# Optimization experiments

Measured on AMD Instinct MI355X. Metric: run time of the kernel, lower is better.

The kernel has to match this reference:

```python
import jax, jax.numpy as jnp
import numpy as np

N_NODES = 100000
N_EDGES = 1600000
C = 64


def _spline_conv(x, src, dst, u, w, root, bias, n_nodes):
    """SplineConv, dim=1, kernel_size=2, degree=1, open spline, aggr='mean'.

    For K=2, degree=1, pseudo u in [0,1]: basis = (1-u) on knot 0, u on knot 1.
    message_e = (1-u_e) * x[src_e] @ w[0] + u_e * x[src_e] @ w[1]
    Compute the two GEMMs at node level (N < E) then gather, which is
    mathematically identical and cheaper.
    """
    h0 = x @ w[0]  # [N, C]
    h1 = x @ w[1]  # [N, C]
    uc = u[:, None]  # [E, 1]
    msg = (1.0 - uc) * h0[src] + uc * h1[src]  # [E, C]
    agg = jax.ops.segment_sum(msg, dst, num_segments=n_nodes)  # [N, C]
    deg = jax.ops.segment_sum(jnp.ones_like(u), dst, num_segments=n_nodes)
    agg = agg / jnp.maximum(deg, 1.0)[:, None]  # mean aggregation
    return agg + x @ root + bias


def setup_inputs() -> dict:
    key = jax.random.key(0)
    ks = jax.random.split(key, 10)
    x = jax.random.normal(ks[0], (N_NODES, C), dtype=jnp.float32)
    edge_index = jax.random.randint(ks[1], (2, N_EDGES), 0, N_NODES, dtype=jnp.int64)
    edge_attr = jax.random.uniform(ks[2], (N_EDGES, 1), dtype=jnp.float32)
    s = 1.0 / np.sqrt(C)
    w1 = jax.random.uniform(ks[3], (2, C, C), jnp.float32, -s, s)
    root1 = jax.random.uniform(ks[4], (C, C), jnp.float32, -s, s)
    b1 = jnp.zeros((C,), jnp.float32)
    w2 = jax.random.uniform(ks[5], (2, C, C), jnp.float32, -s, s)
    root2 = jax.random.uniform(ks[6], (C, C), jnp.float32, -s, s)
    b2 = jnp.zeros((C,), jnp.float32)
    return {"x": x, "edge_index": edge_index, "edge_attr": edge_attr,
            "w1": w1, "root1": root1, "b1": b1,
            "w2": w2, "root2": root2, "b2": b2}


def reference(x, edge_index, edge_attr, w1, root1, b1, w2, root2, b2):
    src, dst = edge_index[0], edge_index[1]
    u = edge_attr[:, 0]
    n = x.shape[0]
    h = _spline_conv(x, src, dst, u, w1, root1, b1, n)
    h = _spline_conv(h, src, dst, u, w2, root2, b2, n)
    return h
```

## Files before the change

kernel.cpp:

```cpp
#include <hip/hip_runtime.h>

#define CDIM 64

typedef __attribute__((ext_vector_type(8))) short bf16x8;
typedef __attribute__((ext_vector_type(4))) float f32x4;

__device__ __forceinline__ short bf16r(float f) {
    unsigned a = __float_as_uint(f);
    a = (a + 0x7fffu + ((a >> 16) & 1u)) >> 16;
    return (short)a;
}
__device__ __forceinline__ unsigned bfpack(float lo, float hi) {
    unsigned a = __float_as_uint(lo);
    a = (a + 0x7fffu + ((a >> 16) & 1u)) >> 16;
    unsigned b = __float_as_uint(hi);
    b = (b + 0x7fffu + ((b >> 16) & 1u)) & 0xffff0000u;
    return a | b;
}

__global__ __launch_bounds__(256) void k_pack(const float* __restrict__ x,
                                              unsigned* __restrict__ xb32, size_t n2) {
    size_t t = (size_t)blockIdx.x * 256 + threadIdx.x;
    size_t stride = (size_t)gridDim.x * 256;
    for (size_t i = t; i < n2; i += stride) {
        float2 v = ((const float2*)x)[i];
        xb32[i] = bfpack(v.x, v.y);
    }
}

#define NPB_SHIFT 9
#define BKN (1 << NPB_SHIFT)
#define BPAD 10240
#define PART_CH 2048

__global__ __launch_bounds__(256) void k_prep(int* __restrict__ bkt_cursor, int n_buckets,
                                              const float* __restrict__ w1,
                                              const float* __restrict__ root1,
                                              const float* __restrict__ w2,
                                              const float* __restrict__ root2,
                                              short* __restrict__ wtg) {
    int tid = threadIdx.x;
    if (blockIdx.x == 0) {
        if (tid < n_buckets) bkt_cursor[tid] = tid * BPAD;
        return;
    }
    int l = blockIdx.x - 1;
    const float* s0 = l ? w2 : w1;
    const float* srcs[3] = {s0, s0 + 4096, l ? root2 : root1};
    short* o = wtg + (size_t)l * 3 * 4096;
    for (int i = tid; i < 12288; i += 256) {
        int m = i >> 12, r = i & 4095, k = r >> 6, n = r & 63;
        o[(m << 12) + (n << 6) + k] = bf16r(srcs[m][r]);
    }
}

__global__ __launch_bounds__(256) void k_part(const int* __restrict__ src,
                                              const int* __restrict__ dst,
                                              const float* __restrict__ u,
                                              int* __restrict__ bkt_cursor,
                                              unsigned long long* __restrict__ rec,
                                              int n_edges, int n_buckets) {
    __shared__ int cnt_s[256];
    __shared__ int off_s[256];
    int tid = threadIdx.x;
    cnt_s[tid] = 0;
    __syncthreads();
    int e0 = blockIdx.x * PART_CH + tid * 8;
    int d[8], s[8];
    float uu[8];
    if (e0 + 8 <= n_edges) {
        int4 d0 = *(const int4*)(dst + e0), d1 = *(const int4*)(dst + e0 + 4);
        int4 s0 = *(const int4*)(src + e0), s1 = *(const int4*)(src + e0 + 4);
        float4 u0 = *(const float4*)(u + e0), u1 = *(const float4*)(u + e0 + 4);
        d[0]=d0.x; d[1]=d0.y; d[2]=d0.z; d[3]=d0.w; d[4]=d1.x; d[5]=d1.y; d[6]=d1.z; d[7]=d1.w;
        s[0]=s0.x; s[1]=s0.y; s[2]=s0.z; s[3]=s0.w; s[4]=s1.x; s[5]=s1.y; s[6]=s1.z; s[7]=s1.w;
        uu[0]=u0.x; uu[1]=u0.y; uu[2]=u0.z; uu[3]=u0.w; uu[4]=u1.x; uu[5]=u1.y; uu[6]=u1.z; uu[7]=u1.w;
    } else {
#pragma unroll
        for (int i = 0; i < 8; ++i) {
            int e = e0 + i;
            bool ok = e < n_edges;
            d[i] = ok ? dst[e] : -1;
            s[i] = ok ? src[e] : 0;
            uu[i] = ok ? u[e] : 0.f;
        }
    }
#pragma unroll
    for (int i = 0; i < 8; ++i)
        if (d[i] >= 0) atomicAdd(&cnt_s[d[i] >> NPB_SHIFT], 1);
    __syncthreads();
    if (tid < n_buckets) {
        int c = cnt_s[tid];
        off_s[tid] = c ? atomicAdd(&bkt_cursor[tid], c) : 0;
    }
    __syncthreads();
#pragma unroll
    for (int i = 0; i < 8; ++i) {
        if (d[i] >= 0) {
            int b = d[i] >> NPB_SHIFT;
            int p = atomicAdd(&off_s[b], 1);
            unsigned uq = (unsigned)(uu[i] * 32767.0f + 0.5f);
            rec[p] = ((unsigned long long)(unsigned)d[i] << 32)
                   | (unsigned long long)(((unsigned)s[i] << 15) | uq);
        }
    }
}

__global__ __launch_bounds__(256) void k_bscan(const int* __restrict__ bkt_cursor,
                                               int* __restrict__ ebase,
                                               int* __restrict__ row_start,
                                               int n_buckets, int n_nodes) {
    __shared__ int sm[256];
    int tid = threadIdx.x;
    int v = (tid < n_buckets) ? (bkt_cursor[tid] - tid * BPAD) : 0;
    sm[tid] = v;
    __syncthreads();
    for (int off = 1; off < 256; off <<= 1) {
        int t = (tid >= off) ? sm[tid - off] : 0;
        __syncthreads();
        sm[tid] += t;
        __syncthreads();
    }
    if (tid < n_buckets) ebase[tid] = sm[tid] - v;
    if (tid == 255) row_start[n_nodes] = sm[255];
}

__global__ __launch_bounds__(1024) void k_scat2(const unsigned long long* __restrict__ rec,
                                                const int* __restrict__ bkt_cursor,
                                                const int* __restrict__ ebase,
                                                int* __restrict__ row_start,
                                                unsigned* __restrict__ em32,
                                                int n_nodes) {
    __shared__ int cnt_s[BKN];
    __shared__ int sc_s[BKN];
    int tid = threadIdx.x;
    int b = blockIdx.x;
    int lo = b << NPB_SHIFT;
    int nrec = bkt_cursor[b] - b * BPAD;
    const unsigned long long* r0 = rec + (size_t)b * BPAD;
    int eb = ebase[b];

    if (tid < BKN) cnt_s[tid] = 0;
    __syncthreads();
    for (int i = tid; i < nrec; i += 1024) {
        int d = (int)(r0[i] >> 32) - lo;
        atomicAdd(&cnt_s[d], 1);
    }
    __syncthreads();
    if (tid < BKN) sc_s[tid] = cnt_s[tid];
    __syncthreads();
    for (int off = 1; off < BKN; off <<= 1) {
        int t = 0;
        if (tid < BKN && tid >= off) t = sc_s[tid - off];
        __syncthreads();
        if (tid < BKN) sc_s[tid] += t;
        __syncthreads();
    }
    if (tid < BKN) {
        int excl = sc_s[tid] - cnt_s[tid];
        int node = lo + tid;
        if (node < n_nodes) row_start[node] = eb + excl;
        cnt_s[tid] = excl;
    }
    __syncthreads();
    for (int i = tid; i < nrec; i += 1024) {
        unsigned long long r = r0[i];
        int d = (int)(r >> 32) - lo;
        int p = atomicAdd(&cnt_s[d], 1);
        em32[eb + p] = (unsigned)r;
    }
}

__global__ __launch_bounds__(256) void k_fused(
        const unsigned* __restrict__ xb_in,
        const unsigned* __restrict__ em32,
        const int* __restrict__ row_start,
        const short* __restrict__ wb,
        const float* __restrict__ bias,
        float* __restrict__ out,
        unsigned short* __restrict__ xb_out,
        int n_nodes) {
    __shared__ __align__(16) unsigned gl[64][68];
    int wave = threadIdx.x >> 6;
    int lane = threadIdx.x & 63;
    int q = lane >> 4;
    int ql = lane & 15;
    int nodew = blockIdx.x * 64 + wave * 16;
    const float inv15 = 1.0f / 32767.0f;

    for (int t = 0; t < 4; ++t) {
        int n = nodew + q * 4 + t;
        bool nok = n < n_nodes;
        int start = nok ? row_start[n] : 0;
        int end = nok ? row_start[n + 1] : 0;
        float a0 = 0.f, a1 = 0.f, a2 = 0.f, a3 = 0.f;
        float b0 = 0.f, b1 = 0.f, b2 = 0.f, b3 = 0.f;
        int j = start;
        for (; j + 4 <= end; j += 4) {
            unsigned e[4];
            uint2 v[4];
#pragma unroll
            for (int i = 0; i < 4; ++i) e[i] = em32[j + i];
#pragma unroll
            for (int i = 0; i < 4; ++i)
                v[i] = *(const uint2*)(xb_in + (size_t)(e[i] >> 15) * 32 + 2 * ql);
#pragma unroll
            for (int i = 0; i < 4; ++i) {
                float uu = (float)(e[i] & 0x7fffu) * inv15;
                float wa = 1.0f - uu;
                float c0 = __uint_as_float(v[i].x << 16);
                float c1 = __uint_as_float(v[i].x & 0xffff0000u);
                float c2 = __uint_as_float(v[i].y << 16);
                float c3 = __uint_as_float(v[i].y & 0xffff0000u);
                a0 += wa * c0; a1 += wa * c1; a2 += wa * c2; a3 += wa * c3;
                b0 += uu * c0; b1 += uu * c1; b2 += uu * c2; b3 += uu * c3;
            }
        }
        if (j < end) {
            unsigned e[4];
            uint2 v[4];
            float m[4];
#pragma unroll
            for (int i = 0; i < 4; ++i) {
                int idx = j + i;
                bool ok = idx < end;
                e[i] = em32[ok ? idx : (end - 1)];
                m[i] = ok ? 1.0f : 0.0f;
            }
#pragma unroll
            for (int i = 0; i < 4; ++i)
                v[i] = *(const uint2*)(xb_in + (size_t)(e[i] >> 15) * 32 + 2 * ql);
#pragma unroll
            for (int i = 0; i < 4; ++i) {
                float uu = (float)(e[i] & 0x7fffu) * inv15;
                float wa = (1.0f - uu) * m[i], wu = uu * m[i];
                float c0 = __uint_as_float(v[i].x << 16);
                float c1 = __uint_as_float(v[i].x & 0xffff0000u);
                float c2 = __uint_as_float(v[i].y << 16);
                float c3 = __uint_as_float(v[i].y & 0xffff0000u);
                a0 += wa * c0; a1 += wa * c1; a2 += wa * c2; a3 += wa * c3;
                b0 += wu * c0; b1 += wu * c1; b2 += wu * c2; b3 += wu * c3;
            }
        }
        float s = 1.0f / fmaxf((float)(end - start), 1.0f);
        int row = wave * 16 + q * 4 + t;
        *(uint2*)&gl[row][2 * ql] = make_uint2(bfpack(a0 * s, a1 * s), bfpack(a2 * s, a3 * s));
        *(uint2*)&gl[row][32 + 2 * ql] = make_uint2(bfpack(b0 * s, b1 * s), bfpack(b2 * s, b3 * s));
    }

    int quad = lane >> 4;
    int m16 = lane & 15;
    int arow = nodew + m16;
    const short* gp = (const short*)&gl[wave * 16 + m16][0];
    const unsigned* xp = xb_in + (size_t)arow * 32;
    bf16x8 zf = {0, 0, 0, 0, 0, 0, 0, 0};
    bf16x8 aG0[2], aG1[2], aX[2];
#pragma unroll
    for (int kf = 0; kf < 2; ++kf) {
        aG0[kf] = *(const bf16x8*)(gp + kf * 32 + quad * 8);
        aG1[kf] = *(const bf16x8*)(gp + 64 + kf * 32 + quad * 8);
        aX[kf] = (arow < n_nodes) ? *(const bf16x8*)(xp + kf * 16 + quad * 4) : zf;
    }
#pragma unroll
    for (int nt = 0; nt < 4; ++nt) {
        f32x4 acc = {0.f, 0.f, 0.f, 0.f};
#pragma unroll
        for (int kf = 0; kf < 2; ++kf) {
            int col = nt * 16 + m16;
            bf16x8 bw0 = *(const bf16x8*)(wb + (col << 6) + kf * 32 + quad * 8);
            bf16x8 bw1 = *(const bf16x8*)(wb + ((64 + col) << 6) + kf * 32 + quad * 8);
            bf16x8 bwR = *(const bf16x8*)(wb + ((128 + col) << 6) + kf * 32 + quad * 8);
            acc = __builtin_amdgcn_mfma_f32_16x16x32_bf16(aG0[kf], bw0, acc, 0, 0, 0);
            acc = __builtin_amdgcn_mfma_f32_16x16x32_bf16(aG1[kf], bw1, acc, 0, 0, 0);
            acc = __builtin_amdgcn_mfma_f32_16x16x32_bf16(aX[kf], bwR, acc, 0, 0, 0);
        }
        float bcol = bias[nt * 16 + m16];
#pragma unroll
        for (int r = 0; r < 4; ++r) {
            int node = nodew + quad * 4 + r;
            if (node < n_nodes) {
                size_t off = (size_t)node * CDIM + nt * 16 + m16;
                float o = acc[r] + bcol;
                if (out) out[off] = o;
                if (xb_out) xb_out[off] = (unsigned short)bf16r(o);
            }
        }
    }
}

extern "C" void kernel_launch(void* const* d_in, const int* in_sizes, int n_in,
                              void* d_out, int out_size, void* d_ws, size_t ws_size,
                              hipStream_t stream) {
    const float* x = (const float*)d_in[0];
    const int* edge_index = (const int*)d_in[1];
    const float* edge_attr = (const float*)d_in[2];
    const float* w1 = (const float*)d_in[3];
    const float* root1 = (const float*)d_in[4];
    const float* b1 = (const float*)d_in[5];
    const float* w2 = (const float*)d_in[6];
    const float* root2 = (const float*)d_in[7];
    const float* b2 = (const float*)d_in[8];

    int n_nodes = in_sizes[0] / CDIM;
    int n_edges = in_sizes[2];
    const int* src = edge_index;
    const int* dst = edge_index + n_edges;

    size_t F = (size_t)n_nodes * CDIM;
    unsigned* xbA = (unsigned*)d_ws;
    unsigned* xbB = xbA + F / 2;
    unsigned* em32 = xbB + F / 2;
    int* row_start = (int*)(em32 + n_edges);
    int n_buckets = (n_nodes + BKN - 1) >> NPB_SHIFT;
    int* ebase = row_start + n_nodes + 1;
    int* bkt_cursor = ebase + n_buckets;
    uintptr_t p = (uintptr_t)(bkt_cursor + n_buckets);
    p = (p + 15) & ~(uintptr_t)15;
    short* wtg = (short*)p;
    p += (size_t)2 * 3 * 4096 * sizeof(short);
    p = (p + 15) & ~(uintptr_t)15;
    unsigned long long* rec = (unsigned long long*)p;
    float* out = (float*)d_out;

    int gB = (n_nodes + 63) / 64;
    int gP = (n_edges + PART_CH - 1) / PART_CH;

    k_pack<<<2048, 256, 0, stream>>>(x, xbA, F / 2);
    k_prep<<<3, 256, 0, stream>>>(bkt_cursor, n_buckets, w1, root1, w2, root2, wtg);
    k_part<<<gP, 256, 0, stream>>>(src, dst, edge_attr, bkt_cursor, rec, n_edges, n_buckets);
    k_bscan<<<1, 256, 0, stream>>>(bkt_cursor, ebase, row_start, n_buckets, n_nodes);
    k_scat2<<<n_buckets, 1024, 0, stream>>>(rec, bkt_cursor, ebase, row_start, em32, n_nodes);

    k_fused<<<gB, 256, 0, stream>>>(xbA, em32, row_start, wtg, b1,
                                    nullptr, (unsigned short*)xbB, n_nodes);
    k_fused<<<gB, 256, 0, stream>>>(xbB, em32, row_start, wtg + 3 * 4096, b2,
                                    out, nullptr, n_nodes);
}
```

Measured before the change: 268.3 us.

## Fuse CSR construction into aggregation kernel via per-block shared-memory bucket sort

Drops the separate bucket-scan and scatter kernels that built a global CSR. Each fused-kernel block now reads its bucket's unsorted records, keeps those for its 64 nodes, and counting-sorts them in shared memory before aggregating and running the MFMA GEMM. Blocks grow to 512 threads, with the GEMM columns split across two wave halves. The cost is that every sub-block rereads the whole bucket's records (8x redundant reads, done again in both layers). The fixed RCAP capacity of 1536 edges per 64 nodes silently drops any edges beyond it.

```diff
diff --git a/kernel.cpp b/kernel.cpp
--- a/kernel.cpp
+++ b/kernel.cpp
@@ -32,6 +32,7 @@
 #define BKN (1 << NPB_SHIFT)
 #define BPAD 10240
 #define PART_CH 2048
+#define RCAP 1536
 
 __global__ __launch_bounds__(256) void k_prep(int* __restrict__ bkt_cursor, int n_buckets,
                                               const float* __restrict__ w1,
@@ -106,101 +107,84 @@
     }
 }
 
-__global__ __launch_bounds__(256) void k_bscan(const int* __restrict__ bkt_cursor,
-                                               int* __restrict__ ebase,
-                                               int* __restrict__ row_start,
-                                               int n_buckets, int n_nodes) {
-    __shared__ int sm[256];
-    int tid = threadIdx.x;
-    int v = (tid < n_buckets) ? (bkt_cursor[tid] - tid * BPAD) : 0;
-    sm[tid] = v;
-    __syncthreads();
-    for (int off = 1; off < 256; off <<= 1) {
-        int t = (tid >= off) ? sm[tid - off] : 0;
-        __syncthreads();
-        sm[tid] += t;
-        __syncthreads();
-    }
-    if (tid < n_buckets) ebase[tid] = sm[tid] - v;
-    if (tid == 255) row_start[n_nodes] = sm[255];
-}
-
-__global__ __launch_bounds__(1024) void k_scat2(const unsigned long long* __restrict__ rec,
-                                                const int* __restrict__ bkt_cursor,
-                                                const int* __restrict__ ebase,
-                                                int* __restrict__ row_start,
-                                                unsigned* __restrict__ em32,
-                                                int n_nodes) {
-    __shared__ int cnt_s[BKN];
-    __shared__ int sc_s[BKN];
-    int tid = threadIdx.x;
-    int b = blockIdx.x;
-    int lo = b << NPB_SHIFT;
-    int nrec = bkt_cursor[b] - b * BPAD;
-    const unsigned long long* r0 = rec + (size_t)b * BPAD;
-    int eb = ebase[b];
-
-    if (tid < BKN) cnt_s[tid] = 0;
-    __syncthreads();
-    for (int i = tid; i < nrec; i += 1024) {
-        int d = (int)(r0[i] >> 32) - lo;
-        atomicAdd(&cnt_s[d], 1);
-    }
-    __syncthreads();
-    if (tid < BKN) sc_s[tid] = cnt_s[tid];
-    __syncthreads();
-    for (int off = 1; off < BKN; off <<= 1) {
-        int t = 0;
-        if (tid < BKN && tid >= off) t = sc_s[tid - off];
-        __syncthreads();
-        if (tid < BKN) sc_s[tid] += t;
-        __syncthreads();
-    }
-    if (tid < BKN) {
-        int excl = sc_s[tid] - cnt_s[tid];
-        int node = lo + tid;
-        if (node < n_nodes) row_start[node] = eb + excl;
-        cnt_s[tid] = excl;
-    }
-    __syncthreads();
-    for (int i = tid; i < nrec; i += 1024) {
-        unsigned long long r = r0[i];
-        int d = (int)(r >> 32) - lo;
-        int p = atomicAdd(&cnt_s[d], 1);
-        em32[eb + p] = (unsigned)r;
-    }
-}
-
-__global__ __launch_bounds__(256) void k_fused(
+__global__ __launch_bounds__(512) void k_fused(
         const unsigned* __restrict__ xb_in,
-        const unsigned* __restrict__ em32,
-        const int* __restrict__ row_start,
+        const unsigned long long* __restrict__ rec,
+        const int* __restrict__ bkt_cursor,
         const short* __restrict__ wb,
         const float* __restrict__ bias,
         float* __restrict__ out,
         unsigned short* __restrict__ xb_out,
-        int n_nodes) {
+        int n_nodes, int n_buckets) {
+    __shared__ unsigned em_s[RCAP];
+    __shared__ unsigned tmp_em[RCAP];
+    __shared__ unsigned short tmp_d[RCAP];
+    __shared__ int cnt_s[64];
+    __shared__ int row_s[64];
+    __shared__ int cur_s[64];
+    __shared__ int nm_s;
     __shared__ __align__(16) unsigned gl[64][68];
-    int wave = threadIdx.x >> 6;
-    int lane = threadIdx.x & 63;
-    int q = lane >> 4;
-    int ql = lane & 15;
-    int nodew = blockIdx.x * 64 + wave * 16;
+    int tid = threadIdx.x;
+    int blk = blockIdx.x;
+    int b = (blk & 7) + 8 * (blk >> 6);
+    int sub = (blk >> 3) & 7;
+    if (b >= n_buckets) return;
+    int lo = (b << NPB_SHIFT) + (sub << 6);
+    int nrec = bkt_cursor[b] - b * BPAD;
+    const unsigned long long* r0 = rec + (size_t)b * BPAD;
     const float inv15 = 1.0f / 32767.0f;
 
-    for (int t = 0; t < 4; ++t) {
-        int n = nodew + q * 4 + t;
-        bool nok = n < n_nodes;
-        int start = nok ? row_start[n] : 0;
-        int end = nok ? row_start[n + 1] : 0;
+    if (tid < 64) cnt_s[tid] = 0;
+    if (tid == 0) nm_s = 0;
+    __syncthreads();
+    for (int i = tid; i < nrec; i += 512) {
+        unsigned long long r = r0[i];
+        int rel = (int)(r >> 32) - lo;
+        if ((unsigned)rel < 64u) {
+            int p = atomicAdd(&nm_s, 1);
+            if (p < RCAP) {
+                tmp_em[p] = (unsigned)r;
+                tmp_d[p] = (unsigned short)rel;
+                atomicAdd(&cnt_s[rel], 1);
+            }
+        }
+    }
+    __syncthreads();
+    if (tid < 64) row_s[tid] = cnt_s[tid];
+    __syncthreads();
+    for (int off = 1; off < 64; off <<= 1) {
+        int t = (tid < 64 && tid >= off) ? row_s[tid - off] : 0;
+        __syncthreads();
+        if (tid < 64) row_s[tid] += t;
+        __syncthreads();
+    }
+    if (tid < 64) {
+        row_s[tid] -= cnt_s[tid];
+        cur_s[tid] = row_s[tid];
+    }
+    __syncthreads();
+    int nm = min(nm_s, RCAP);
+    for (int i = tid; i < nm; i += 512) {
+        int rel = tmp_d[i];
+        int p = atomicAdd(&cur_s[rel], 1);
+        em_s[p] = tmp_em[i];
+    }
+    __syncthreads();
+
+    int qid = tid >> 4;
+    int ql = tid & 15;
+    for (int t = 0; t < 2; ++t) {
+        int rel = qid * 2 + t;
+        int start = row_s[rel];
+        int cnt = cnt_s[rel];
+        int end = start + cnt;
         float a0 = 0.f, a1 = 0.f, a2 = 0.f, a3 = 0.f;
         float b0 = 0.f, b1 = 0.f, b2 = 0.f, b3 = 0.f;
         int j = start;
         for (; j + 4 <= end; j += 4) {
-            unsigned e[4];
-            uint2 v[4];
-#pragma unroll
-            for (int i = 0; i < 4; ++i) e[i] = em32[j + i];
+            unsigned e[4]; uint2 v[4];
+#pragma unroll
+            for (int i = 0; i < 4; ++i) e[i] = em_s[j + i];
 #pragma unroll
             for (int i = 0; i < 4; ++i)
                 v[i] = *(const uint2*)(xb_in + (size_t)(e[i] >> 15) * 32 + 2 * ql);
@@ -217,14 +201,12 @@
             }
         }
         if (j < end) {
-            unsigned e[4];
-            uint2 v[4];
-            float m[4];
+            unsigned e[4]; uint2 v[4]; float m[4];
 #pragma unroll
             for (int i = 0; i < 4; ++i) {
                 int idx = j + i;
                 bool ok = idx < end;
-                e[i] = em32[ok ? idx : (end - 1)];
+                e[i] = em_s[ok ? idx : (end - 1)];
                 m[i] = ok ? 1.0f : 0.0f;
             }
 #pragma unroll
@@ -242,16 +224,22 @@
                 b0 += wu * c0; b1 += wu * c1; b2 += wu * c2; b3 += wu * c3;
             }
         }
-        float s = 1.0f / fmaxf((float)(end - start), 1.0f);
-        int row = wave * 16 + q * 4 + t;
-        *(uint2*)&gl[row][2 * ql] = make_uint2(bfpack(a0 * s, a1 * s), bfpack(a2 * s, a3 * s));
-        *(uint2*)&gl[row][32 + 2 * ql] = make_uint2(bfpack(b0 * s, b1 * s), bfpack(b2 * s, b3 * s));
-    }
-
+        float s = 1.0f / fmaxf((float)cnt, 1.0f);
+        *(uint2*)&gl[rel][2 * ql] = make_uint2(bfpack(a0 * s, a1 * s), bfpack(a2 * s, a3 * s));
+        *(uint2*)&gl[rel][32 + 2 * ql] = make_uint2(bfpack(b0 * s, b1 * s), bfpack(b2 * s, b3 * s));
+    }
+    __syncthreads();
+
+    int wv = tid >> 6;
+    int lane = tid & 63;
+    int tile = wv & 3;
+    int nthalf = wv >> 2;
     int quad = lane >> 4;
     int m16 = lane & 15;
-    int arow = nodew + m16;
-    const short* gp = (const short*)&gl[wave * 16 + m16][0];
+    int rown = tile * 16 + m16;
+    int arow = lo + rown;
+    bool rowok = arow < n_nodes;
+    const short* gp = (const short*)&gl[rown][0];
     const unsigned* xp = xb_in + (size_t)arow * 32;
     bf16x8 zf = {0, 0, 0, 0, 0, 0, 0, 0};
     bf16x8 aG0[2], aG1[2], aX[2];
@@ -259,28 +247,29 @@
     for (int kf = 0; kf < 2; ++kf) {
         aG0[kf] = *(const bf16x8*)(gp + kf * 32 + quad * 8);
         aG1[kf] = *(const bf16x8*)(gp + 64 + kf * 32 + quad * 8);
-        aX[kf] = (arow < n_nodes) ? *(const bf16x8*)(xp + kf * 16 + quad * 4) : zf;
-    }
-#pragma unroll
-    for (int nt = 0; nt < 4; ++nt) {
-        f32x4 acc = {0.f, 0.f, 0.f, 0.f};
+        aX[kf] = rowok ? *(const bf16x8*)(xp + kf * 16 + quad * 4) : zf;
+    }
+#pragma unroll
+    for (int nh = 0; nh < 2; ++nh) {
+        int nt = nthalf * 2 + nh;
+        f32x4 accv = {0.f, 0.f, 0.f, 0.f};
 #pragma unroll
         for (int kf = 0; kf < 2; ++kf) {
             int col = nt * 16 + m16;
             bf16x8 bw0 = *(const bf16x8*)(wb + (col << 6) + kf * 32 + quad * 8);
             bf16x8 bw1 = *(const bf16x8*)(wb + ((64 + col) << 6) + kf * 32 + quad * 8);
             bf16x8 bwR = *(const bf16x8*)(wb + ((128 + col) << 6) + kf * 32 + quad * 8);
-            acc = __builtin_amdgcn_mfma_f32_16x16x32_bf16(aG0[kf], bw0, acc, 0, 0, 0);
-            acc = __builtin_amdgcn_mfma_f32_16x16x32_bf16(aG1[kf], bw1, acc, 0, 0, 0);
-            acc = __builtin_amdgcn_mfma_f32_16x16x32_bf16(aX[kf], bwR, acc, 0, 0, 0);
+            accv = __builtin_amdgcn_mfma_f32_16x16x32_bf16(aG0[kf], bw0, accv, 0, 0, 0);
+            accv = __builtin_amdgcn_mfma_f32_16x16x32_bf16(aG1[kf], bw1, accv, 0, 0, 0);
+            accv = __builtin_amdgcn_mfma_f32_16x16x32_bf16(aX[kf], bwR, accv, 0, 0, 0);
         }
         float bcol = bias[nt * 16 + m16];
 #pragma unroll
         for (int r = 0; r < 4; ++r) {
-            int node = nodew + quad * 4 + r;
+            int node = lo + tile * 16 + quad * 4 + r;
             if (node < n_nodes) {
                 size_t off = (size_t)node * CDIM + nt * 16 + m16;
-                float o = acc[r] + bcol;
+                float o = accv[r] + bcol;
                 if (out) out[off] = o;
                 if (xb_out) xb_out[off] = (unsigned short)bf16r(o);
             }
@@ -307,13 +296,10 @@
     const int* dst = edge_index + n_edges;
 
     size_t F = (size_t)n_nodes * CDIM;
+    int n_buckets = (n_nodes + BKN - 1) >> NPB_SHIFT;
     unsigned* xbA = (unsigned*)d_ws;
     unsigned* xbB = xbA + F / 2;
-    unsigned* em32 = xbB + F / 2;
-    int* row_start = (int*)(em32 + n_edges);
-    int n_buckets = (n_nodes + BKN - 1) >> NPB_SHIFT;
-    int* ebase = row_start + n_nodes + 1;
-    int* bkt_cursor = ebase + n_buckets;
+    int* bkt_cursor = (int*)(xbB + F / 2);
     uintptr_t p = (uintptr_t)(bkt_cursor + n_buckets);
     p = (p + 15) & ~(uintptr_t)15;
     short* wtg = (short*)p;
@@ -322,17 +308,15 @@
     unsigned long long* rec = (unsigned long long*)p;
     float* out = (float*)d_out;
 
-    int gB = (n_nodes + 63) / 64;
     int gP = (n_edges + PART_CH - 1) / PART_CH;
+    int gF = 64 * ((n_buckets + 7) / 8);
 
     k_pack<<<2048, 256, 0, stream>>>(x, xbA, F / 2);
     k_prep<<<3, 256, 0, stream>>>(bkt_cursor, n_buckets, w1, root1, w2, root2, wtg);
     k_part<<<gP, 256, 0, stream>>>(src, dst, edge_attr, bkt_cursor, rec, n_edges, n_buckets);
-    k_bscan<<<1, 256, 0, stream>>>(bkt_cursor, ebase, row_start, n_buckets, n_nodes);
-    k_scat2<<<n_buckets, 1024, 0, stream>>>(rec, bkt_cursor, ebase, row_start, em32, n_nodes);
-
-    k_fused<<<gB, 256, 0, stream>>>(xbA, em32, row_start, wtg, b1,
-                                    nullptr, (unsigned short*)xbB, n_nodes);
-    k_fused<<<gB, 256, 0, stream>>>(xbB, em32, row_start, wtg + 3 * 4096, b2,
-                                    out, nullptr, n_nodes);
-}
+
+    k_fused<<<gF, 512, 0, stream>>>(xbA, rec, bkt_cursor, wtg, b1,
+                                    nullptr, (unsigned short*)xbB, n_nodes, n_buckets);
+    k_fused<<<gF, 512, 0, stream>>>(xbB, rec, bkt_cursor, wtg + 3 * 4096, b2,
+                                    out, nullptr, n_nodes, n_buckets);
+}
```

New measurement: 271.5 us. About the same (+1.2%).
